# Kernel tuning notes

Measured on AMD Instinct MI355X. Metric: run time of the kernel, lower is better.

## Reference

```python
import jax, jax.numpy as jnp
import numpy as np

B, T, K = 128, 2048, 64
GAMMA = 2.0


def setup_inputs() -> dict:
    key = jax.random.key(0)
    k1, k2, k3, k4, k5 = jax.random.split(key, 5)
    emissions = jax.random.normal(k1, (B, T, K), dtype=jnp.float32)
    labels = jax.random.randint(k2, (B, T), 0, K)
    mask = jnp.ones((B, T), dtype=bool)
    transitions = jax.random.normal(k3, (K, K), dtype=jnp.float32) * 0.1
    start_transitions = jax.random.normal(k4, (K,), dtype=jnp.float32) * 0.1
    end_transitions = jax.random.normal(k5, (K,), dtype=jnp.float32) * 0.1
    return dict(emissions=emissions, labels=labels, mask=mask,
                transitions=transitions, start_transitions=start_transitions,
                end_transitions=end_transitions)


def _crf_llh(emissions, tags, mask, trans, start, end):
    # torchcrf-style log-likelihood per sequence (batch_first layout)
    Bm = emissions.shape[0]
    brange = jnp.arange(Bm)
    fmask = mask.astype(emissions.dtype)
    # time-major slices for the scan over t = 1..T-1
    em_seq = jnp.swapaxes(emissions, 0, 1)[1:]   # [T-1, B, K]
    tag_seq = tags.T[1:]                          # [T-1, B]
    m_seq = fmask.T[1:]                           # [T-1, B]

    # ---- gold-path (numerator) score ----
    score0 = start[tags[:, 0]] + emissions[brange, 0, tags[:, 0]]

    def num_step(carry, xs):
        prev_tag, score = carry
        em_t, tag_t, m_t = xs
        step = trans[prev_tag, tag_t] + em_t[brange, tag_t]
        score = score + step * m_t
        prev_tag = jnp.where(m_t > 0, tag_t, prev_tag)
        return (prev_tag, score), None

    (last_tag, score), _ = jax.lax.scan(num_step, (tags[:, 0], score0),
                                        (em_seq, tag_seq, m_seq))
    score = score + end[last_tag]

    # ---- log-partition (denominator) via forward algorithm ----
    alpha0 = start[None, :] + emissions[:, 0]  # [B, K]

    def part_step(alpha, xs):
        em_t, m_t = xs
        # [B, K_prev, K_next] logsumexp over previous tag
        nxt = jax.nn.logsumexp(alpha[:, :, None] + trans[None, :, :] + em_t[:, None, :], axis=1)
        alpha = jnp.where((m_t > 0)[:, None], nxt, alpha)
        return alpha, None

    alpha, _ = jax.lax.scan(part_step, alpha0, (em_seq, m_seq))
    logZ = jax.nn.logsumexp(alpha + end[None, :], axis=1)
    return score - logZ  # [B]


def reference(emissions, labels, mask, transitions, start_transitions, end_transitions):
    crf_labels = jnp.where(labels == -100, 0, labels)
    valid_mask = (labels != -100) & mask
    llh = _crf_llh(emissions, crf_labels, valid_mask,
                   transitions, start_transitions, end_transitions)
    crf_loss = -jnp.mean(llh)  # torchcrf reduction='mean' = mean over batch

    # focal scale computed with no grad
    logp = jax.nn.log_softmax(emissions, axis=-1)
    p_t = jnp.exp(jnp.take_along_axis(logp, crf_labels[..., None], axis=-1))[..., 0]
    focal_weight = (1.0 - p_t) ** GAMMA
    vm = valid_mask.astype(emissions.dtype)
    focal_scale = jnp.sum(focal_weight * vm) / jnp.maximum(jnp.sum(vm), 1.0)
    focal_scale = jnp.maximum(focal_scale, 0.1)
    focal_scale = jax.lax.stop_gradient(focal_scale)
    return crf_loss * focal_scale
```

## Files before the change

### kernel.cpp

```cpp
#include <hip/hip_runtime.h>

#define B_ 128
#define T_ 2048
#define K_ 64
#define C_ 8
#define S_ 256
#define NSCAN (B_*C_)
#define NF_ 256
#define L2E 1.44269504088896340736f
#define LN2 0.69314718055994530942f

#define POFF 0
#define LOFF (NSCAN*4096)
#define GOFF (LOFF + NSCAN)
#define LLOFF (GOFF + B_)
#define FOFF (LLOFF + B_)

typedef __attribute__((ext_vector_type(4))) unsigned int uint4v;
typedef __attribute__((ext_vector_type(8))) short short8v;
typedef __attribute__((ext_vector_type(16))) float f32x16;
typedef __attribute__((ext_vector_type(4))) float float4v;

__device__ __forceinline__ float rfl_f(float x) {
    return __int_as_float(__builtin_amdgcn_readfirstlane(__float_as_int(x)));
}
__device__ __forceinline__ unsigned pkbf16(float lo, float hi) {
    unsigned r;
    asm volatile("v_cvt_pk_bf16_f32 %0, %1, %2" : "=v"(r) : "v"(lo), "v"(hi));
    return r;
}
__device__ __forceinline__ short8v mk8(unsigned a, unsigned b, unsigned c, unsigned d) {
    uint4v u; u[0] = a; u[1] = b; u[2] = c; u[3] = d;
    return __builtin_bit_cast(short8v, u);
}
__device__ __forceinline__ f32x16 zero16() {
    f32x16 z;
    #pragma unroll
    for (int i = 0; i < 16; ++i) z[i] = 0.f;
    return z;
}

__global__ __launch_bounds__(64, 1) void fcrf_scan(
    const float* __restrict__ em, const int* __restrict__ lab,
    const int* __restrict__ msk, const float* __restrict__ trans,
    const float* __restrict__ stv, const float* __restrict__ env,
    float* __restrict__ ws)
{
    __shared__ float sh[K_ * K_];
    const int lane = threadIdx.x;
    const int blk = blockIdx.x;
    const int h = lane >> 5;
    const int cc = lane & 31;

    if (blk < NSCAN) {
        const int w = blk, b = w >> 3, c = w & 7;
        const float* emB = em + (size_t)b * T_ * K_;
        const int* labB = lab + (size_t)b * T_;
        const int* mskB = msk + (size_t)b * T_;

        unsigned au[2][4][4];
        #pragma unroll
        for (int I = 0; I < 2; ++I)
            #pragma unroll
            for (int s = 0; s < 4; ++s) {
                float wv[8];
                #pragma unroll
                for (int j = 0; j < 8; ++j)
                    wv[j] = __builtin_amdgcn_exp2f(
                        trans[(16*s + 8*h + j) * K_ + 32*I + cc] * L2E);
                #pragma unroll
                for (int p = 0; p < 4; ++p)
                    au[I][s][p] = pkbf16(wv[2*p], wv[2*p+1]);
            }

        unsigned bu[4][2][4];
        #pragma unroll
        for (int s = 0; s < 4; ++s)
            #pragma unroll
            for (int J = 0; J < 2; ++J)
                #pragma unroll
                for (int p = 0; p < 4; ++p) {
                    int k0 = 16*s + 8*h + 2*p, col = 32*J + cc;
                    unsigned u = 0;
                    if (k0 == col) u |= 0x3F80u;
                    if (k0 + 1 == col) u |= 0x3F800000u;
                    bu[s][J][p] = u;
                }

        float L = 0.f;
        int t = 1 + c * S_;
        float4v er[2][4];
        int lc, mc2;
        {
            int tl = t < T_ ? t : T_ - 1;
            const float4v* ep = (const float4v*)(emB + (size_t)tl * K_);
            #pragma unroll
            for (int I = 0; I < 2; ++I)
                #pragma unroll
                for (int Q = 0; Q < 4; ++Q) er[I][Q] = ep[8*I + 2*Q + h];
            lc = labB[tl]; mc2 = mskB[tl];
        }

        for (int st = 0; st < S_; ++st) {
            int tn = t + 1;
            int tln = tn < T_ ? tn : T_ - 1;
            float4v en[2][4];
            const float4v* epn = (const float4v*)(emB + (size_t)tln * K_);
            #pragma unroll
            for (int I = 0; I < 2; ++I)
                #pragma unroll
                for (int Q = 0; Q < 4; ++Q) en[I][Q] = epn[8*I + 2*Q + h];
            int ln_ = labB[tln], mn_ = mskB[tln];

            bool m = (t < T_) && (lc != -100) && (mc2 != 0);
            if (m) {
                f32x16 acc[2][2];
                #pragma unroll
                for (int I = 0; I < 2; ++I)
                    #pragma unroll
                    for (int J = 0; J < 2; ++J) acc[I][J] = zero16();
                #pragma unroll
                for (int s = 0; s < 4; ++s) {
                    short8v bs0 = mk8(bu[s][0][0], bu[s][0][1], bu[s][0][2], bu[s][0][3]);
                    short8v bs1 = mk8(bu[s][1][0], bu[s][1][1], bu[s][1][2], bu[s][1][3]);
                    short8v as0 = mk8(au[0][s][0], au[0][s][1], au[0][s][2], au[0][s][3]);
                    short8v as1 = mk8(au[1][s][0], au[1][s][1], au[1][s][2], au[1][s][3]);
                    acc[0][0] = __builtin_amdgcn_mfma_f32_32x32x16_bf16(as0, bs0, acc[0][0], 0, 0, 0);
                    acc[0][1] = __builtin_amdgcn_mfma_f32_32x32x16_bf16(as0, bs1, acc[0][1], 0, 0, 0);
                    acc[1][0] = __builtin_amdgcn_mfma_f32_32x32x16_bf16(as1, bs0, acc[1][0], 0, 0, 0);
                    acc[1][1] = __builtin_amdgcn_mfma_f32_32x32x16_bf16(as1, bs1, acc[1][1], 0, 0, 0);
                }
                float c00 = rfl_f(acc[0][0][0]);
                float rho = __builtin_amdgcn_rcpf(c00);
                L += __builtin_amdgcn_logf(c00) * LN2;
                float fr[2][4][4];
                #pragma unroll
                for (int I = 0; I < 2; ++I)
                    #pragma unroll
                    for (int Q = 0; Q < 4; ++Q)
                        #pragma unroll
                        for (int e = 0; e < 4; ++e)
                            fr[I][Q][e] = __builtin_amdgcn_exp2f(er[I][Q][e] * L2E) * rho;
                #pragma unroll
                for (int I = 0; I < 2; ++I)
                    #pragma unroll
                    for (int J = 0; J < 2; ++J) {
                        float sc[16];
                        #pragma unroll
                        for (int r = 0; r < 16; ++r)
                            sc[r] = acc[I][J][r] * fr[I][r >> 2][r & 3];
                        #pragma unroll
                        for (int sg = 0; sg < 2; ++sg) {
                            const int s = 2*I + sg;
                            const int r0 = 8*sg;
                            unsigned X  = pkbf16(sc[r0+0], sc[r0+1]);
                            unsigned X2 = pkbf16(sc[r0+2], sc[r0+3]);
                            unsigned Y  = pkbf16(sc[r0+4], sc[r0+5]);
                            unsigned Y2 = pkbf16(sc[r0+6], sc[r0+7]);
                            unsigned sX  = (unsigned)__shfl_xor((int)X,  32, 64);
                            unsigned sX2 = (unsigned)__shfl_xor((int)X2, 32, 64);
                            unsigned sY  = (unsigned)__shfl_xor((int)Y,  32, 64);
                            unsigned sY2 = (unsigned)__shfl_xor((int)Y2, 32, 64);
                            bu[s][J][0] = h ? sY  : X;
                            bu[s][J][1] = h ? sY2 : X2;
                            bu[s][J][2] = h ? Y   : sX;
                            bu[s][J][3] = h ? Y2  : sX2;
                        }
                    }
            }
            #pragma unroll
            for (int I = 0; I < 2; ++I)
                #pragma unroll
                for (int Q = 0; Q < 4; ++Q) er[I][Q] = en[I][Q];
            lc = ln_; mc2 = mn_;
            ++t;
        }
        float* pw = ws + POFF + (size_t)w * 4096;
        #pragma unroll
        for (int s = 0; s < 4; ++s)
            #pragma unroll
            for (int J = 0; J < 2; ++J)
                #pragma unroll
                for (int p = 0; p < 4; ++p) {
                    unsigned u = bu[s][J][p];
                    int k0 = 16*s + 8*h + 2*p, col = 32*J + cc;
                    pw[k0 * 64 + col] = __uint_as_float(u << 16);
                    pw[(k0 + 1) * 64 + col] = __uint_as_float(u & 0xFFFF0000u);
                }
        if (lane == 0) ws[LOFF + w] = L;
    } else if (blk < NSCAN + B_) {
        const int b = blk - NSCAN;
        const int* labB = lab + (size_t)b * T_;
        const int* mskB = msk + (size_t)b * T_;
        for (int i = 0; i < K_; ++i) sh[i * K_ + lane] = trans[i * K_ + lane];
        __syncthreads();
        float sacc = 0.f;
        int carry = 0;
        for (int it = 0; it < T_ / 64; ++it) {
            int tt = it * 64 + lane;
            int lb = labB[tt], mk = mskB[tt];
            int tg = (lb == -100) ? 0 : lb;
            int vm = (lb != -100) && (mk != 0);
            unsigned long long bal = __ballot(vm || tt == 0);
            if (bal == ~0ull) {
                int prev = __shfl_up(tg, 1, 64);
                if (lane == 0) prev = carry;
                float term;
                if (tt == 0)
                    term = stv[tg] + em[(size_t)b * T_ * K_ + tg];
                else
                    term = vm ? (sh[prev * K_ + tg] + em[((size_t)b * T_ + tt) * K_ + tg]) : 0.f;
                sacc += term;
                carry = __builtin_amdgcn_readlane(tg, 63);
            } else {
                int cl = carry;
                float sl = 0.f;
                if (lane == 0) {
                    for (int u = 0; u < 64; ++u) {
                        int t2 = it * 64 + u;
                        int lb2 = labB[t2], mk2 = mskB[t2];
                        int tg2 = (lb2 == -100) ? 0 : lb2;
                        int vm2 = (lb2 != -100) && (mk2 != 0);
                        if (t2 == 0) { sl += stv[tg2] + em[(size_t)b * T_ * K_ + tg2]; cl = tg2; }
                        else if (vm2) { sl += sh[cl * K_ + tg2] + em[((size_t)b * T_ + t2) * K_ + tg2]; cl = tg2; }
                    }
                }
                sacc += sl;
                carry = __builtin_amdgcn_readlane(cl, 0);
            }
        }
        if (lane == 0) sacc += env[carry];
        #pragma unroll
        for (int off = 1; off < 64; off <<= 1) sacc += __shfl_xor(sacc, off, 64);
        if (lane == 0) ws[GOFF + b] = sacc;
    } else {
        const int fb = blk - NSCAN - B_;
        const float4* em4 = (const float4*)em;
        const int sub = lane >> 4;
        const int cg = lane & 15;
        float facc = 0.f, cacc = 0.f;
        const int base = fb * (B_ * T_ / NF_);
        for (int it = 0; it < (B_ * T_ / NF_) / 4; ++it) {
            int row = base + it * 4 + sub;
            float4 v = em4[row * (K_ / 4) + cg];
            int lb = lab[row];
            int vm = (lb != -100) & (msk[row] != 0);
            int tg = (lb == -100) ? 0 : lb;
            float mx = fmaxf(fmaxf(v.x, v.y), fmaxf(v.z, v.w));
            #pragma unroll
            for (int off = 1; off < 16; off <<= 1) mx = fmaxf(mx, __shfl_xor(mx, off, 64));
            float se = __builtin_amdgcn_exp2f((v.x - mx) * L2E)
                     + __builtin_amdgcn_exp2f((v.y - mx) * L2E)
                     + __builtin_amdgcn_exp2f((v.z - mx) * L2E)
                     + __builtin_amdgcn_exp2f((v.w - mx) * L2E);
            int c0 = cg * 4;
            float sel = ((c0 + 0 == tg) ? v.x : 0.f) + ((c0 + 1 == tg) ? v.y : 0.f)
                      + ((c0 + 2 == tg) ? v.z : 0.f) + ((c0 + 3 == tg) ? v.w : 0.f);
            #pragma unroll
            for (int off = 1; off < 16; off <<= 1) {
                se += __shfl_xor(se, off, 64);
                sel += __shfl_xor(sel, off, 64);
            }
            float p = __builtin_amdgcn_exp2f((sel - mx) * L2E) / se;
            float fw = (1.f - p) * (1.f - p);
            if (cg == 0) {
                facc += vm ? fw : 0.f;
                cacc += vm ? 1.f : 0.f;
            }
        }
        #pragma unroll
        for (int off = 1; off < 64; off <<= 1) {
            facc += __shfl_xor(facc, off, 64);
            cacc += __shfl_xor(cacc, off, 64);
        }
        if (lane == 0) {
            ws[FOFF + 2 * fb] = facc;
            ws[FOFF + 2 * fb + 1] = cacc;
        }
    }
}

__global__ __launch_bounds__(64) void fcrf_combine(
    const float* __restrict__ em, const float* __restrict__ stv,
    const float* __restrict__ env, float* __restrict__ ws)
{
    __shared__ __align__(16) float vb[64];
    const int b = blockIdx.x, j = threadIdx.x;
    float a = stv[j] + em[(size_t)b * T_ * K_ + j];
    float a0 = rfl_f(a);
    float Lv = a0;
    float v = __builtin_amdgcn_exp2f((a - a0) * L2E);
    for (int c = 0; c < C_; ++c) {
        vb[j] = v;
        __syncthreads();
        const float4v* gp = (const float4v*)(ws + POFF + (size_t)(b * C_ + c) * 4096 + j * 64);
        const float4v* vp = (const float4v*)vb;
        float s0 = 0.f, s1 = 0.f, s2 = 0.f, s3 = 0.f;
        #pragma unroll
        for (int q = 0; q < 16; ++q) {
            float4v g = gp[q];
            float4v x = vp[q];
            s0 = fmaf(g[0], x[0], s0);
            s1 = fmaf(g[1], x[1], s1);
            s2 = fmaf(g[2], x[2], s2);
            s3 = fmaf(g[3], x[3], s3);
        }
        float out = (s0 + s1) + (s2 + s3);
        float o0 = rfl_f(out);
        v = out * __builtin_amdgcn_rcpf(o0);
        Lv += __builtin_amdgcn_logf(o0) * LN2 + ws[LOFF + b * C_ + c];
        __syncthreads();
    }
    float x = v * __builtin_amdgcn_exp2f(env[j] * L2E);
    #pragma unroll
    for (int off = 1; off < 64; off <<= 1) x += __shfl_xor(x, off, 64);
    float logZ = Lv + __builtin_amdgcn_logf(x) * LN2;
    if (j == 0) ws[LLOFF + b] = ws[GOFF + b] - logZ;
}

__global__ __launch_bounds__(64) void fcrf_final(const float* __restrict__ ws,
                                                 float* __restrict__ out)
{
    const int lane = threadIdx.x;
    float llh = ws[LLOFF + lane] + ws[LLOFF + 64 + lane];
    float f = 0.f, c = 0.f;
    #pragma unroll
    for (int k = 0; k < NF_ / 64; ++k) {
        int i = lane + 64 * k;
        f += ws[FOFF + 2 * i];
        c += ws[FOFF + 2 * i + 1];
    }
    #pragma unroll
    for (int off = 1; off < 64; off <<= 1) {
        llh += __shfl_xor(llh, off, 64);
        f += __shfl_xor(f, off, 64);
        c += __shfl_xor(c, off, 64);
    }
    if (lane == 0) {
        float crf = -(llh * (1.0f / B_));
        float scale = f / fmaxf(c, 1.f);
        scale = fmaxf(scale, 0.1f);
        out[0] = crf * scale;
    }
}

extern "C" void kernel_launch(void* const* d_in, const int* in_sizes, int n_in,
                              void* d_out, int out_size, void* d_ws, size_t ws_size,
                              hipStream_t stream) {
    const float* em = (const float*)d_in[0];
    const int* lab = (const int*)d_in[1];
    const int* msk = (const int*)d_in[2];
    const float* trans = (const float*)d_in[3];
    const float* stv = (const float*)d_in[4];
    const float* env = (const float*)d_in[5];
    float* ws = (float*)d_ws;
    float* out = (float*)d_out;

    fcrf_scan<<<dim3(NSCAN + B_ + NF_), dim3(64), 0, stream>>>(em, lab, msk, trans, stv, env, ws);
    fcrf_combine<<<dim3(B_), dim3(64), 0, stream>>>(em, stv, env, ws);
    fcrf_final<<<dim3(1), dim3(64), 0, stream>>>(ws, out);
}
```

Measured before the change: 372.3 us.

## Split CRF scan into more chunks, reorder MFMAs, store bf16 partial products

Doubles the number of time chunks per sequence and halves the chunk length, so the serial per-chunk matrix-product chain is shorter and more waves run in parallel (launch bounds now allow 2 waves). The MFMA chain for the first accumulator is issued first so the normaliser log and exp can overlap with the remaining MFMAs, and normalisation is folded into the exp argument. Cross-half shuffles become permlane32 swaps, and chunk transfer matrices are written as packed bf16, which halves workspace traffic and makes the combine kernel unpack them. The gold-path block reads transitions from global memory instead of LDS. The cost is a longer serial combine loop and extra bf16 unpacking.

```diff
diff --git a/kernel.cpp b/kernel.cpp
--- a/kernel.cpp
+++ b/kernel.cpp
@@ -3,19 +3,19 @@
 #define B_ 128
 #define T_ 2048
 #define K_ 64
-#define C_ 8
-#define S_ 256
+#define C_ 16
+#define S_ 128
 #define NSCAN (B_*C_)
 #define NF_ 256
 #define L2E 1.44269504088896340736f
 #define LN2 0.69314718055994530942f
 
-#define POFF 0
-#define LOFF (NSCAN*4096)
+#define LOFF (NSCAN*2048)
 #define GOFF (LOFF + NSCAN)
 #define LLOFF (GOFF + B_)
 #define FOFF (LLOFF + B_)
 
+typedef __attribute__((ext_vector_type(2))) unsigned int uint2v;
 typedef __attribute__((ext_vector_type(4))) unsigned int uint4v;
 typedef __attribute__((ext_vector_type(8))) short short8v;
 typedef __attribute__((ext_vector_type(16))) float f32x16;
@@ -29,36 +29,33 @@
     asm volatile("v_cvt_pk_bf16_f32 %0, %1, %2" : "=v"(r) : "v"(lo), "v"(hi));
     return r;
 }
+__device__ __forceinline__ void swap32(unsigned &x, unsigned &y) {
+    uint2v r = __builtin_amdgcn_permlane32_swap(x, y, false, false);
+    x = r[0]; y = r[1];
+}
 __device__ __forceinline__ short8v mk8(unsigned a, unsigned b, unsigned c, unsigned d) {
     uint4v u; u[0] = a; u[1] = b; u[2] = c; u[3] = d;
     return __builtin_bit_cast(short8v, u);
 }
-__device__ __forceinline__ f32x16 zero16() {
-    f32x16 z;
-    #pragma unroll
-    for (int i = 0; i < 16; ++i) z[i] = 0.f;
-    return z;
-}
-
-__global__ __launch_bounds__(64, 1) void fcrf_scan(
+
+__global__ __launch_bounds__(64, 2) void fcrf_scan(
     const float* __restrict__ em, const int* __restrict__ lab,
     const int* __restrict__ msk, const float* __restrict__ trans,
     const float* __restrict__ stv, const float* __restrict__ env,
     float* __restrict__ ws)
 {
-    __shared__ float sh[K_ * K_];
     const int lane = threadIdx.x;
     const int blk = blockIdx.x;
     const int h = lane >> 5;
     const int cc = lane & 31;
 
     if (blk < NSCAN) {
-        const int w = blk, b = w >> 3, c = w & 7;
+        const int w = blk, b = w >> 4, c = w & 15;
         const float* emB = em + (size_t)b * T_ * K_;
         const int* labB = lab + (size_t)b * T_;
         const int* mskB = msk + (size_t)b * T_;
 
-        unsigned au[2][4][4];
+        short8v as8[2][4];
         #pragma unroll
         for (int I = 0; I < 2; ++I)
             #pragma unroll
@@ -68,12 +65,11 @@
                 for (int j = 0; j < 8; ++j)
                     wv[j] = __builtin_amdgcn_exp2f(
                         trans[(16*s + 8*h + j) * K_ + 32*I + cc] * L2E);
-                #pragma unroll
-                for (int p = 0; p < 4; ++p)
-                    au[I][s][p] = pkbf16(wv[2*p], wv[2*p+1]);
-            }
-
-        unsigned bu[4][2][4];
+                as8[I][s] = mk8(pkbf16(wv[0], wv[1]), pkbf16(wv[2], wv[3]),
+                                pkbf16(wv[4], wv[5]), pkbf16(wv[6], wv[7]));
+            }
+
+        uint4v bu4[4][2];
         #pragma unroll
         for (int s = 0; s < 4; ++s)
             #pragma unroll
@@ -84,21 +80,24 @@
                     unsigned u = 0;
                     if (k0 == col) u |= 0x3F80u;
                     if (k0 + 1 == col) u |= 0x3F800000u;
-                    bu[s][J][p] = u;
+                    bu4[s][J][p] = u;
                 }
+
+        f32x16 ZR;
+        #pragma unroll
+        for (int i = 0; i < 16; ++i) ZR[i] = 0.f;
 
         float L = 0.f;
         int t = 1 + c * S_;
         float4v er[2][4];
         int lc, mc2;
         {
-            int tl = t < T_ ? t : T_ - 1;
-            const float4v* ep = (const float4v*)(emB + (size_t)tl * K_);
+            const float4v* ep = (const float4v*)(emB + (size_t)t * K_);
             #pragma unroll
             for (int I = 0; I < 2; ++I)
                 #pragma unroll
                 for (int Q = 0; Q < 4; ++Q) er[I][Q] = ep[8*I + 2*Q + h];
-            lc = labB[tl]; mc2 = mskB[tl];
+            lc = labB[t]; mc2 = mskB[t];
         }
 
         for (int st = 0; st < S_; ++st) {
@@ -114,25 +113,23 @@
 
             bool m = (t < T_) && (lc != -100) && (mc2 != 0);
             if (m) {
-                f32x16 acc[2][2];
-                #pragma unroll
-                for (int I = 0; I < 2; ++I)
-                    #pragma unroll
-                    for (int J = 0; J < 2; ++J) acc[I][J] = zero16();
-                #pragma unroll
-                for (int s = 0; s < 4; ++s) {
-                    short8v bs0 = mk8(bu[s][0][0], bu[s][0][1], bu[s][0][2], bu[s][0][3]);
-                    short8v bs1 = mk8(bu[s][1][0], bu[s][1][1], bu[s][1][2], bu[s][1][3]);
-                    short8v as0 = mk8(au[0][s][0], au[0][s][1], au[0][s][2], au[0][s][3]);
-                    short8v as1 = mk8(au[1][s][0], au[1][s][1], au[1][s][2], au[1][s][3]);
-                    acc[0][0] = __builtin_amdgcn_mfma_f32_32x32x16_bf16(as0, bs0, acc[0][0], 0, 0, 0);
-                    acc[0][1] = __builtin_amdgcn_mfma_f32_32x32x16_bf16(as0, bs1, acc[0][1], 0, 0, 0);
-                    acc[1][0] = __builtin_amdgcn_mfma_f32_32x32x16_bf16(as1, bs0, acc[1][0], 0, 0, 0);
-                    acc[1][1] = __builtin_amdgcn_mfma_f32_32x32x16_bf16(as1, bs1, acc[1][1], 0, 0, 0);
-                }
-                float c00 = rfl_f(acc[0][0][0]);
-                float rho = __builtin_amdgcn_rcpf(c00);
-                L += __builtin_amdgcn_logf(c00) * LN2;
+                short8v b00 = __builtin_bit_cast(short8v, bu4[0][0]);
+                short8v b10 = __builtin_bit_cast(short8v, bu4[1][0]);
+                short8v b20 = __builtin_bit_cast(short8v, bu4[2][0]);
+                short8v b30 = __builtin_bit_cast(short8v, bu4[3][0]);
+                short8v b01 = __builtin_bit_cast(short8v, bu4[0][1]);
+                short8v b11 = __builtin_bit_cast(short8v, bu4[1][1]);
+                short8v b21 = __builtin_bit_cast(short8v, bu4[2][1]);
+                short8v b31 = __builtin_bit_cast(short8v, bu4[3][1]);
+
+                f32x16 a00 = __builtin_amdgcn_mfma_f32_32x32x16_bf16(as8[0][0], b00, ZR, 0, 0, 0);
+                a00 = __builtin_amdgcn_mfma_f32_32x32x16_bf16(as8[0][1], b10, a00, 0, 0, 0);
+                a00 = __builtin_amdgcn_mfma_f32_32x32x16_bf16(as8[0][2], b20, a00, 0, 0, 0);
+                a00 = __builtin_amdgcn_mfma_f32_32x32x16_bf16(as8[0][3], b30, a00, 0, 0, 0);
+                float c00 = rfl_f(a00[0]);
+                float lg = __builtin_amdgcn_logf(c00);
+                L = fmaf(lg, LN2, L);
+                float nlg = -lg;
                 float fr[2][4][4];
                 #pragma unroll
                 for (int I = 0; I < 2; ++I)
@@ -140,33 +137,46 @@
                     for (int Q = 0; Q < 4; ++Q)
                         #pragma unroll
                         for (int e = 0; e < 4; ++e)
-                            fr[I][Q][e] = __builtin_amdgcn_exp2f(er[I][Q][e] * L2E) * rho;
-                #pragma unroll
-                for (int I = 0; I < 2; ++I)
-                    #pragma unroll
-                    for (int J = 0; J < 2; ++J) {
-                        float sc[16];
-                        #pragma unroll
-                        for (int r = 0; r < 16; ++r)
-                            sc[r] = acc[I][J][r] * fr[I][r >> 2][r & 3];
-                        #pragma unroll
-                        for (int sg = 0; sg < 2; ++sg) {
-                            const int s = 2*I + sg;
-                            const int r0 = 8*sg;
-                            unsigned X  = pkbf16(sc[r0+0], sc[r0+1]);
-                            unsigned X2 = pkbf16(sc[r0+2], sc[r0+3]);
-                            unsigned Y  = pkbf16(sc[r0+4], sc[r0+5]);
-                            unsigned Y2 = pkbf16(sc[r0+6], sc[r0+7]);
-                            unsigned sX  = (unsigned)__shfl_xor((int)X,  32, 64);
-                            unsigned sX2 = (unsigned)__shfl_xor((int)X2, 32, 64);
-                            unsigned sY  = (unsigned)__shfl_xor((int)Y,  32, 64);
-                            unsigned sY2 = (unsigned)__shfl_xor((int)Y2, 32, 64);
-                            bu[s][J][0] = h ? sY  : X;
-                            bu[s][J][1] = h ? sY2 : X2;
-                            bu[s][J][2] = h ? Y   : sX;
-                            bu[s][J][3] = h ? Y2  : sX2;
-                        }
+                            fr[I][Q][e] = __builtin_amdgcn_exp2f(
+                                fmaf(er[I][Q][e], L2E, nlg));
+
+                f32x16 a01 = __builtin_amdgcn_mfma_f32_32x32x16_bf16(as8[0][0], b01, ZR, 0, 0, 0);
+                a01 = __builtin_amdgcn_mfma_f32_32x32x16_bf16(as8[0][1], b11, a01, 0, 0, 0);
+                a01 = __builtin_amdgcn_mfma_f32_32x32x16_bf16(as8[0][2], b21, a01, 0, 0, 0);
+                a01 = __builtin_amdgcn_mfma_f32_32x32x16_bf16(as8[0][3], b31, a01, 0, 0, 0);
+                f32x16 a10 = __builtin_amdgcn_mfma_f32_32x32x16_bf16(as8[1][0], b00, ZR, 0, 0, 0);
+                a10 = __builtin_amdgcn_mfma_f32_32x32x16_bf16(as8[1][1], b10, a10, 0, 0, 0);
+                a10 = __builtin_amdgcn_mfma_f32_32x32x16_bf16(as8[1][2], b20, a10, 0, 0, 0);
+                a10 = __builtin_amdgcn_mfma_f32_32x32x16_bf16(as8[1][3], b30, a10, 0, 0, 0);
+                f32x16 a11 = __builtin_amdgcn_mfma_f32_32x32x16_bf16(as8[1][0], b01, ZR, 0, 0, 0);
+                a11 = __builtin_amdgcn_mfma_f32_32x32x16_bf16(as8[1][1], b11, a11, 0, 0, 0);
+                a11 = __builtin_amdgcn_mfma_f32_32x32x16_bf16(as8[1][2], b21, a11, 0, 0, 0);
+                a11 = __builtin_amdgcn_mfma_f32_32x32x16_bf16(as8[1][3], b31, a11, 0, 0, 0);
+
+                #define PACKQ(I, J, ACC)                                              \
+                    {                                                                  \
+                        _Pragma("unroll")                                              \
+                        for (int sg = 0; sg < 2; ++sg) {                               \
+                            const int r0 = 8 * sg, s2 = 2 * (I) + sg;                  \
+                            unsigned X  = pkbf16((ACC)[r0+0]*fr[I][2*sg][0],           \
+                                                 (ACC)[r0+1]*fr[I][2*sg][1]);          \
+                            unsigned X2 = pkbf16((ACC)[r0+2]*fr[I][2*sg][2],           \
+                                                 (ACC)[r0+3]*fr[I][2*sg][3]);          \
+                            unsigned Y  = pkbf16((ACC)[r0+4]*fr[I][2*sg+1][0],         \
+                                                 (ACC)[r0+5]*fr[I][2*sg+1][1]);        \
+                            unsigned Y2 = pkbf16((ACC)[r0+6]*fr[I][2*sg+1][2],         \
+                                                 (ACC)[r0+7]*fr[I][2*sg+1][3]);        \
+                            swap32(X, Y);                                              \
+                            swap32(X2, Y2);                                            \
+                            bu4[s2][J][0] = X;  bu4[s2][J][1] = X2;                    \
+                            bu4[s2][J][2] = Y;  bu4[s2][J][3] = Y2;                    \
+                        }                                                              \
                     }
+                PACKQ(0, 0, a00)
+                PACKQ(0, 1, a01)
+                PACKQ(1, 0, a10)
+                PACKQ(1, 1, a11)
+                #undef PACKQ
             }
             #pragma unroll
             for (int I = 0; I < 2; ++I)
@@ -175,25 +185,20 @@
             lc = ln_; mc2 = mn_;
             ++t;
         }
-        float* pw = ws + POFF + (size_t)w * 4096;
+
+        unsigned* pw = (unsigned*)ws + (size_t)w * 2048;
         #pragma unroll
         for (int s = 0; s < 4; ++s)
             #pragma unroll
             for (int J = 0; J < 2; ++J)
                 #pragma unroll
-                for (int p = 0; p < 4; ++p) {
-                    unsigned u = bu[s][J][p];
-                    int k0 = 16*s + 8*h + 2*p, col = 32*J + cc;
-                    pw[k0 * 64 + col] = __uint_as_float(u << 16);
-                    pw[(k0 + 1) * 64 + col] = __uint_as_float(u & 0xFFFF0000u);
-                }
+                for (int p = 0; p < 4; ++p)
+                    pw[(8*s + 4*h + p) * 64 + 32*J + cc] = bu4[s][J][p];
         if (lane == 0) ws[LOFF + w] = L;
     } else if (blk < NSCAN + B_) {
         const int b = blk - NSCAN;
         const int* labB = lab + (size_t)b * T_;
         const int* mskB = msk + (size_t)b * T_;
-        for (int i = 0; i < K_; ++i) sh[i * K_ + lane] = trans[i * K_ + lane];
-        __syncthreads();
         float sacc = 0.f;
         int carry = 0;
         for (int it = 0; it < T_ / 64; ++it) {
@@ -209,7 +214,7 @@
                 if (tt == 0)
                     term = stv[tg] + em[(size_t)b * T_ * K_ + tg];
                 else
-                    term = vm ? (sh[prev * K_ + tg] + em[((size_t)b * T_ + tt) * K_ + tg]) : 0.f;
+                    term = vm ? (trans[prev * K_ + tg] + em[((size_t)b * T_ + tt) * K_ + tg]) : 0.f;
                 sacc += term;
                 carry = __builtin_amdgcn_readlane(tg, 63);
             } else {
@@ -222,7 +227,7 @@
                         int tg2 = (lb2 == -100) ? 0 : lb2;
                         int vm2 = (lb2 != -100) && (mk2 != 0);
                         if (t2 == 0) { sl += stv[tg2] + em[(size_t)b * T_ * K_ + tg2]; cl = tg2; }
-                        else if (vm2) { sl += sh[cl * K_ + tg2] + em[((size_t)b * T_ + t2) * K_ + tg2]; cl = tg2; }
+                        else if (vm2) { sl += trans[cl * K_ + tg2] + em[((size_t)b * T_ + t2) * K_ + tg2]; cl = tg2; }
                     }
                 }
                 sacc += sl;
@@ -284,8 +289,10 @@
     const float* __restrict__ em, const float* __restrict__ stv,
     const float* __restrict__ env, float* __restrict__ ws)
 {
-    __shared__ __align__(16) float vb[64];
+    __shared__ float vb[64];
     const int b = blockIdx.x, j = threadIdx.x;
+    const int rp = j >> 1;
+    const bool hi = (j & 1) != 0;
     float a = stv[j] + em[(size_t)b * T_ * K_ + j];
     float a0 = rfl_f(a);
     float Lv = a0;
@@ -293,28 +300,32 @@
     for (int c = 0; c < C_; ++c) {
         vb[j] = v;
         __syncthreads();
-        const float4v* gp = (const float4v*)(ws + POFF + (size_t)(b * C_ + c) * 4096 + j * 64);
-        const float4v* vp = (const float4v*)vb;
+        const uint4v* gp = (const uint4v*)((const unsigned*)ws
+                             + (size_t)(b * C_ + c) * 2048 + rp * 64);
         float s0 = 0.f, s1 = 0.f, s2 = 0.f, s3 = 0.f;
         #pragma unroll
         for (int q = 0; q < 16; ++q) {
-            float4v g = gp[q];
-            float4v x = vp[q];
-            s0 = fmaf(g[0], x[0], s0);
-            s1 = fmaf(g[1], x[1], s1);
-            s2 = fmaf(g[2], x[2], s2);
-            s3 = fmaf(g[3], x[3], s3);
+            uint4v g = gp[q];
+            unsigned u0 = g[0], u1 = g[1], u2 = g[2], u3 = g[3];
+            float g0 = __uint_as_float(hi ? (u0 & 0xFFFF0000u) : (u0 << 16));
+            float g1 = __uint_as_float(hi ? (u1 & 0xFFFF0000u) : (u1 << 16));
+            float g2 = __uint_as_float(hi ? (u2 & 0xFFFF0000u) : (u2 << 16));
+            float g3 = __uint_as_float(hi ? (u3 & 0xFFFF0000u) : (u3 << 16));
+            s0 = fmaf(g0, vb[4*q + 0], s0);
+            s1 = fmaf(g1, vb[4*q + 1], s1);
+            s2 = fmaf(g2, vb[4*q + 2], s2);
+            s3 = fmaf(g3, vb[4*q + 3], s3);
         }
         float out = (s0 + s1) + (s2 + s3);
         float o0 = rfl_f(out);
         v = out * __builtin_amdgcn_rcpf(o0);
-        Lv += __builtin_amdgcn_logf(o0) * LN2 + ws[LOFF + b * C_ + c];
+        Lv = fmaf(__builtin_amdgcn_logf(o0), LN2, Lv) + ws[LOFF + b * C_ + c];
         __syncthreads();
     }
     float x = v * __builtin_amdgcn_exp2f(env[j] * L2E);
     #pragma unroll
     for (int off = 1; off < 64; off <<= 1) x += __shfl_xor(x, off, 64);
-    float logZ = Lv + __builtin_amdgcn_logf(x) * LN2;
+    float logZ = fmaf(__builtin_amdgcn_logf(x), LN2, Lv);
     if (j == 0) ws[LLOFF + b] = ws[GOFF + b] - logZ;
 }
 
```

Measured after the change: 411.1 us. 10.4% more time.
